# Kernel optimization log

Hardware: AMD Instinct MI355X
Metric: run time of the kernel (lower is better)

The kernel has to match this reference:

```python
import jax, jax.numpy as jnp
import numpy as np

N_NODES = 10000
N_EDGES = 320000
MUL = 32            # multiplicity of each input/output irrep
RADIAL = 8          # edge scalar (radial basis) dim
HID = 64            # fc_neurons widths
NUM_NEIGHBORS = 32.0
MIX = np.pi / 8.0
INV_SQRT2 = 1.0 / np.sqrt(2.0)   # per-path alpha: 2 paths feed each mid irrep
INV_SQRT3 = 1.0 / np.sqrt(3.0)   # w3j(1,1,0) normalization


def setup_inputs() -> dict:
    key = jax.random.key(0)
    ks = jax.random.split(key, 16)
    inp = {
        "node_input": jax.random.normal(ks[0], (N_NODES, 4 * MUL), jnp.float32),  # 32x0e+32x1o flat
        "edge_attr": jax.random.normal(ks[1], (N_EDGES, 4), jnp.float32),          # 1x0e+1x1o (sh l=0,1)
        "edge_scalar_attr": jax.random.uniform(ks[2], (N_EDGES, RADIAL), jnp.float32),
        # first linear: 32x0e+32x1o -> (32x0e+32x1o) + (32x0e+32x1o); columns [:MUL]=conv path, [MUL:]=self path
        "W1_0e": jax.random.normal(ks[3], (MUL, 2 * MUL), jnp.float32),
        "W1_1o": jax.random.normal(ks[4], (MUL, 2 * MUL), jnp.float32),
        # radial MLP
        "W_mlp1": jax.random.normal(ks[5], (RADIAL, HID), jnp.float32),
        "W_mlp2": jax.random.normal(ks[6], (HID, HID), jnp.float32),
        # per-instruction 'uvu' path weights (mul_v = 1 squeezed): shape (HID, MUL)
        "Wp_00": jax.random.normal(ks[7], (HID, MUL), jnp.float32),  # 0e x 0e -> 0e
        "Wp_01": jax.random.normal(ks[8], (HID, MUL), jnp.float32),  # 0e x 1o -> 1o
        "Wp_10": jax.random.normal(ks[9], (HID, MUL), jnp.float32),  # 1o x 0e -> 1o
        "Wp_11": jax.random.normal(ks[10], (HID, MUL), jnp.float32), # 1o x 1o -> 0e
        # final linear: 64x0e+64x1o -> 32x0e+32x1o
        "W2_0e": jax.random.normal(ks[11], (2 * MUL, MUL), jnp.float32),
        "W2_1o": jax.random.normal(ks[12], (2 * MUL, MUL), jnp.float32),
        "edge_src": jax.random.randint(ks[13], (N_EDGES,), 0, N_NODES, jnp.int32),
        "edge_dst": jax.random.randint(ks[14], (N_EDGES,), 0, N_NODES, jnp.int32),
    }
    return inp


def _forward(node_input, edge_attr, edge_scalar_attr,
             W1_0e, W1_1o, W_mlp1, W_mlp2,
             Wp_00, Wp_01, Wp_10, Wp_11, W2_0e, W2_1o,
             edge_src, edge_dst):
    N = node_input.shape[0]
    # split flat node features into irrep blocks: 32x0e (N,32), 32x1o (N,32,3)
    x0 = node_input[:, :MUL]
    x1 = node_input[:, MUL:].reshape(N, MUL, 3)

    # ---- equivariant Linear: input -> input + output (fan-in normalized) ----
    f0 = (x0 @ W1_0e) / np.sqrt(MUL)                           # (N, 2*MUL)
    f1 = jnp.einsum('nui,uw->nwi', x1, W1_1o) / np.sqrt(MUL)   # (N, 2*MUL, 3)
    feat0, self0 = f0[:, :MUL], f0[:, MUL:]
    feat1, self1 = f1[:, :MUL], f1[:, MUL:]

    # ---- gather to edges ----
    e0 = feat0[edge_src]        # (E, MUL)
    e1 = feat1[edge_src]        # (E, MUL, 3)
    ea0 = edge_attr[:, :1]      # (E, 1) 0e
    ea1 = edge_attr[:, 1:4]     # (E, 3) 1o

    # ---- radial MLP -> per-edge per-path weights ----
    h = jax.nn.gelu((edge_scalar_attr @ W_mlp1) / np.sqrt(RADIAL))
    h = jax.nn.gelu((h @ W_mlp2) / np.sqrt(HID))               # (E, HID)
    w00 = h @ Wp_00   # (E, MUL)
    w01 = h @ Wp_01
    w10 = h @ Wp_10
    w11 = h @ Wp_11

    # ---- CG tensor product, 'uvu' mode (mul_v = 1) ----
    out0_a = w00 * e0 * ea0                                   # 0e x 0e -> 0e   (E, MUL)
    out0_b = w11 * jnp.sum(e1 * ea1[:, None, :], -1) * INV_SQRT3  # 1o.1o -> 0e
    out1_a = (w01 * e0)[:, :, None] * ea1[:, None, :]         # 0e x 1o -> 1o   (E, MUL, 3)
    out1_b = (w10[:, :, None] * e1) * ea0[:, :, None]         # 1o x 0e -> 1o
    mid0 = jnp.concatenate([out0_a, out0_b], axis=1) * INV_SQRT2  # (E, 2*MUL)   64x0e
    mid1 = jnp.concatenate([out1_a, out1_b], axis=1) * INV_SQRT2  # (E, 2*MUL, 3) 64x1o

    # ---- scatter-add to destination nodes ----
    n0 = jax.ops.segment_sum(mid0, edge_dst, num_segments=N) / np.sqrt(NUM_NEIGHBORS)
    n1 = jax.ops.segment_sum(mid1, edge_dst, num_segments=N) / np.sqrt(NUM_NEIGHBORS)

    # ---- final equivariant Linear: 64x0e+64x1o -> 32x0e+32x1o ----
    conv0 = (n0 @ W2_0e) / np.sqrt(2 * MUL)                    # (N, MUL)
    conv1 = jnp.einsum('nui,uw->nwi', n1, W2_1o) / np.sqrt(2 * MUL)  # (N, MUL, 3)

    c, s = np.cos(MIX), np.sin(MIX)
    y0 = c * self0 + s * conv0
    y1 = c * self1 + s * conv1
    return jnp.concatenate([y0, y1.reshape(N, MUL * 3)], axis=1)  # (N, 128)


def reference(node_input, edge_attr, edge_scalar_attr,
              W1_0e, W1_1o, W_mlp1, W_mlp2,
              Wp_00, Wp_01, Wp_10, Wp_11, W2_0e, W2_1o,
              edge_src, edge_dst):
    return _forward(node_input, edge_attr, edge_scalar_attr,
                    W1_0e, W1_1o, W_mlp1, W_mlp2,
                    Wp_00, Wp_01, Wp_10, Wp_11, W2_0e, W2_1o,
                    edge_src, edge_dst)
```

## Files before the change

### kernel.cpp

```cpp
#include <hip/hip_runtime.h>

typedef unsigned int uint32;
typedef unsigned short ushrt;
typedef __attribute__((ext_vector_type(4))) float f32x4;
typedef __attribute__((ext_vector_type(16))) float f32x16;
typedef __attribute__((ext_vector_type(2))) float f32x2;
typedef __attribute__((ext_vector_type(8))) _Float16 halfx8;
typedef __attribute__((ext_vector_type(4))) uint32 uint32x4;

#define N_NODES 10000
#define N_EDGES 320000

#define SC_W1      0.17677669529663687f
#define SC_MLP1    0.35355339059327373f
#define SC_MLP2    0.125f
#define INV_SQRT3  0.5773502691896258f
#define COS_MIX    0.9238795325112867f
#define SIN_CONV   0.04783542904563623f

#define WS_FEATP 0
#define I_CNT    1280000
#define I_OFF    1290016
#define U_REC    1300032
#define U_WF     2580032
#define U_WBUF   2587200

__device__ __forceinline__ uint32 f2bf(float x) {
    uint32 u = __float_as_uint(x);
    return (u + 0x7fffu + ((u >> 16) & 1u)) >> 16;
}
__device__ __forceinline__ uint32 pack_bf2(float a, float b) {
    return f2bf(a) | (f2bf(b) << 16);
}
__device__ __forceinline__ uint32 packh2(float a, float b) {
    _Float16 ha = (_Float16)a, hb = (_Float16)b;
    return (uint32)__builtin_bit_cast(unsigned short, ha) |
           ((uint32)__builtin_bit_cast(unsigned short, hb) << 16);
}
__device__ __forceinline__ unsigned short h16(float x) {
    _Float16 h = (_Float16)x;
    return __builtin_bit_cast(unsigned short, h);
}
__device__ __forceinline__ unsigned short pack_fp8_2(float a, float b) {
    return (unsigned short)(__builtin_amdgcn_cvt_pk_fp8_f32(a, b, 0, false) & 0xffff);
}
__device__ __forceinline__ float gelu_fast(float x) {
    float x2 = x * x;
    float z = x * __builtin_fmaf(0.03567740814f, x2, 0.7978845608f);
    float E = __builtin_amdgcn_exp2f(z * -2.885390082f);
    return x * __builtin_amdgcn_rcpf(1.0f + E);
}

#define K1_CNT_BLOCKS  1250
#define K1_PREP_BLOCKS 7
__global__ __launch_bounds__(256) void k1_fused(
        const int* __restrict__ edge_dst, int* __restrict__ cnt,
        const float* __restrict__ Wm1, const float* __restrict__ Wm2,
        const float* __restrict__ Wp00, const float* __restrict__ Wp01,
        const float* __restrict__ Wp10, const float* __restrict__ Wp11,
        uint32* __restrict__ wf) {
    int b = blockIdx.x;
    if (b < K1_CNT_BLOCKS) {
        int e = b * 256 + threadIdx.x;
        atomicAdd(&cnt[edge_dst[e]], 1);
    } else {
        int gid = (b - K1_CNT_BLOCKS) * 256 + threadIdx.x;
        if (gid >= 26 * 64) return;
        int f = gid >> 6, lane = gid & 63;
        int kb = (lane >> 5) * 8;
        int c31 = lane & 31;
        float vals[8];
        if (f < 2) {
            int c = 32 * f + c31;
#pragma unroll
            for (int j = 0; j < 8; ++j) { int k = kb + j; vals[j] = (k < 8) ? Wm1[k * 64 + c] : 0.f; }
        } else if (f < 10) {
            int idx = f - 2, nc = idx >> 2, ks = idx & 3;
            int c = 32 * nc + c31;
#pragma unroll
            for (int j = 0; j < 8; ++j) { int k = 16 * ks + kb + j; vals[j] = Wm2[k * 64 + c]; }
        } else {
            int idx = f - 10, m = idx >> 2, ks = idx & 3;
            const float* W = (m == 0) ? Wp00 : (m == 1) ? Wp01 : (m == 2) ? Wp10 : Wp11;
            float sc = (m == 3) ? 0.125f * INV_SQRT3 : 0.125f;
#pragma unroll
            for (int j = 0; j < 8; ++j) { int k = 16 * ks + kb + j; vals[j] = W[k * 32 + c31] * sc; }
        }
        uint32* o = wf + f * 256 + lane * 4;
#pragma unroll
        for (int w = 0; w < 4; ++w) o[w] = packh2(vals[2 * w], vals[2 * w + 1]);
    }
}

__global__ __launch_bounds__(1024) void csr_scan(const int* __restrict__ cnt,
                                                 int* __restrict__ off) {
    __shared__ int partial[1024];
    int t = threadIdx.x;
    const int CHUNK = 10;
    int base = t * CHUNK;
    int s = 0;
#pragma unroll
    for (int j = 0; j < CHUNK; ++j) {
        int idx = base + j;
        s += (idx < N_NODES) ? cnt[idx] : 0;
    }
    partial[t] = s;
    __syncthreads();
    for (int o = 1; o < 1024; o <<= 1) {
        int v = partial[t];
        int add = (t >= o) ? partial[t - o] : 0;
        __syncthreads();
        partial[t] = v + add;
        __syncthreads();
    }
    int run = (t > 0) ? partial[t - 1] : 0;
    for (int j = 0; j < CHUNK; ++j) {
        int idx = base + j;
        if (idx < N_NODES) {
            off[idx] = run;
            run += cnt[idx];
        }
    }
    if (t == 1023) off[N_NODES] = run;
}

#define MLP_BLOCKS 1250
#define K3_NODE_BLOCKS 2500
__global__ __launch_bounds__(256, 3) void k3_fused(
        const float* __restrict__ edge_scalar, const float* __restrict__ edge_attr,
        const int* __restrict__ src_in, const int* __restrict__ dst_in,
        int* __restrict__ off,
        const uint32* __restrict__ wf,
        uint32* __restrict__ wbuf, uint4* __restrict__ rec,
        const float* __restrict__ x,
        const float* __restrict__ W1_0e, const float* __restrict__ W1_1o,
        float* __restrict__ featp, float* __restrict__ out) {
    __shared__ uint32x4 wfl[26 * 64];
    __shared__ unsigned short sh[4][2048];
    __shared__ float eaxs[4][32];
    __shared__ float xrow[4][128];

    int lane = threadIdx.x & 63;
    int wvq = threadIdx.x >> 6;

    if (blockIdx.x >= MLP_BLOCKS) {
        int node = (blockIdx.x - MLP_BLOCKS) * 4 + wvq;
        float2 v = *(const float2*)(x + (size_t)node * 128 + lane * 2);
        xrow[wvq][lane * 2]     = v.x;
        xrow[wvq][lane * 2 + 1] = v.y;
        __syncthreads();
        const float* sx = xrow[wvq];
        int w = lane;
        float f0 = 0.f, f1x = 0.f, f1y = 0.f, f1z = 0.f;
#pragma unroll
        for (int u = 0; u < 32; ++u) {
            float w0 = W1_0e[u * 64 + w];
            float w1 = W1_1o[u * 64 + w];
            f0  += sx[u] * w0;
            f1x += sx[32 + u * 3 + 0] * w1;
            f1y += sx[32 + u * 3 + 1] * w1;
            f1z += sx[32 + u * 3 + 2] * w1;
        }
        f0 *= SC_W1; f1x *= SC_W1; f1y *= SC_W1; f1z *= SC_W1;
        if (w < 32) {
            featp[node * 128 + w]      = f0;
            featp[node * 128 + 32 + w] = f1x;
            featp[node * 128 + 64 + w] = f1y;
            featp[node * 128 + 96 + w] = f1z;
        } else {
            int ww = w - 32;
            out[node * 128 + ww] = COS_MIX * f0;
            out[node * 128 + 32 + ww * 3 + 0] = COS_MIX * f1x;
            out[node * 128 + 32 + ww * 3 + 1] = COS_MIX * f1y;
            out[node * 128 + 32 + ww * 3 + 2] = COS_MIX * f1z;
        }
        return;
    }

    {
        const uint32x4* s = (const uint32x4*)wf;
        for (int i = threadIdx.x; i < 26 * 64; i += 256) wfl[i] = s[i];
    }
    __syncthreads();

    int wave_id = blockIdx.x * 4 + wvq;
    int l31 = lane & 31;
    int lhi = lane >> 5;

    const f32x16 z16 = {0,0,0,0,0,0,0,0,0,0,0,0,0,0,0,0};
    unsigned short* shw = sh[wvq];
    uint32* obw = (uint32*)shw;
    unsigned short* obw16 = shw;

    for (int g = wave_id; g < N_EDGES / 32; g += MLP_BLOCKS * 4) {
        int e0 = g * 32;

        halfx8 a0 = (halfx8)0;
        if (lane < 32) {
            int e = e0 + lane;
            const float* esp = edge_scalar + (size_t)e * 8;
            float4 p = *(const float4*)esp;
            float4 q = *(const float4*)(esp + 4);
            float4 av = *(const float4*)(edge_attr + (size_t)e * 4);
            int dn = dst_in[e];
            int sn = src_in[e];
            int pos = atomicAdd(&off[dn], 1);
            eaxs[wvq][lane] = av.x;
            uint4 rv;
            rv.x = pack_bf2(av.y, av.z);
            rv.y = __float_as_uint(av.w);
            rv.z = (uint32)e;
            rv.w = (uint32)sn;
            rec[pos] = rv;
            a0[0] = (_Float16)p.x; a0[1] = (_Float16)p.y;
            a0[2] = (_Float16)p.z; a0[3] = (_Float16)p.w;
            a0[4] = (_Float16)q.x; a0[5] = (_Float16)q.y;
            a0[6] = (_Float16)q.z; a0[7] = (_Float16)q.w;
        }

        f32x16 acc1[2];
#pragma unroll
        for (int nc = 0; nc < 2; ++nc) {
            halfx8 bb = __builtin_bit_cast(halfx8, wfl[nc * 64 + lane]);
            acc1[nc] = __builtin_amdgcn_mfma_f32_32x32x16_f16(a0, bb, z16, 0, 0, 0);
        }
#pragma unroll
        for (int nc = 0; nc < 2; ++nc)
#pragma unroll
            for (int reg = 0; reg < 16; ++reg) {
                float gv = gelu_fast(acc1[nc][reg] * SC_MLP1);
                int r = (reg & 3) + 8 * (reg >> 2) + 4 * lhi;
                int ix = r * 64 + 32 * nc + l31;
                shw[ix ^ ((r & 7) << 3)] = h16(gv);
            }
        halfx8 a1[4];
#pragma unroll
        for (int ks = 0; ks < 4; ++ks) {
            int ix = l31 * 64 + 16 * ks + lhi * 8;
            a1[ks] = __builtin_bit_cast(halfx8,
                       *(const uint32x4*)&shw[ix ^ ((lane & 7) << 3)]);
        }

        f32x16 acc2[2];
#pragma unroll
        for (int nc = 0; nc < 2; ++nc) {
            acc2[nc] = z16;
#pragma unroll
            for (int ks = 0; ks < 4; ++ks) {
                halfx8 bb = __builtin_bit_cast(halfx8, wfl[(2 + nc * 4 + ks) * 64 + lane]);
                acc2[nc] = __builtin_amdgcn_mfma_f32_32x32x16_f16(a1[ks], bb, acc2[nc], 0, 0, 0);
            }
        }
#pragma unroll
        for (int nc = 0; nc < 2; ++nc)
#pragma unroll
            for (int reg = 0; reg < 16; ++reg) {
                float gv = gelu_fast(acc2[nc][reg] * SC_MLP2);
                int r = (reg & 3) + 8 * (reg >> 2) + 4 * lhi;
                int ix = r * 64 + 32 * nc + l31;
                shw[ix ^ ((r & 7) << 3)] = h16(gv);
            }
        halfx8 a2[4];
#pragma unroll
        for (int ks = 0; ks < 4; ++ks) {
            int ix = l31 * 64 + 16 * ks + lhi * 8;
            a2[ks] = __builtin_bit_cast(halfx8,
                       *(const uint32x4*)&shw[ix ^ ((lane & 7) << 3)]);
        }

        f32x16 accp[4];
#pragma unroll
        for (int m = 0; m < 4; ++m) {
            accp[m] = z16;
#pragma unroll
            for (int ks = 0; ks < 4; ++ks) {
                halfx8 bb = __builtin_bit_cast(halfx8, wfl[(10 + m * 4 + ks) * 64 + lane]);
                accp[m] = __builtin_amdgcn_mfma_f32_32x32x16_f16(a2[ks], bb, accp[m], 0, 0, 0);
            }
        }

#pragma unroll
        for (int reg = 0; reg < 16; ++reg) {
            int r = (reg & 3) + 8 * (reg >> 2) + 4 * lhi;
            float eax = eaxs[wvq][r];
            obw16[r * 64 + l31]      = pack_fp8_2(accp[0][reg] * eax, accp[1][reg]);
            obw16[r * 64 + 32 + l31] = pack_fp8_2(accp[2][reg] * eax, accp[3][reg]);
        }
#pragma unroll
        for (int pass = 0; pass < 4; ++pass) {
            int r = pass * 8 + (lane >> 3);
            int c4 = (lane & 7) * 4;
            uint32x4 v = *(const uint32x4*)&obw[r * 32 + c4];
            *(uint32x4*)(wbuf + (size_t)(e0 + r) * 32 + c4) = v;
        }
    }
}

__global__ __launch_bounds__(256) void gather(const int* __restrict__ off,
                                              const int* __restrict__ cnt,
                                              const uint4* __restrict__ rec,
                                              const uint32* __restrict__ wbuf,
                                              const float* __restrict__ featp,
                                              const float* __restrict__ W2_0e,
                                              const float* __restrict__ W2_1o,
                                              float* __restrict__ out) {
    int wv = threadIdx.x >> 6;
    int lane = threadIdx.x & 63;
    int node = blockIdx.x * 4 + wv;
    int u = lane & 31;
    int half = lane >> 5;

    int end = __builtin_amdgcn_readfirstlane(off[node]);
    int beg = end - __builtin_amdgcn_readfirstlane(cnt[node]);

    float a0acc = 0.f, a1x = 0.f, a1y = 0.f, a1z = 0.f;
    int offA = u + half * 32, offB = 64 + u, offC = 96 + u;
    const ushrt* wbuf16 = (const ushrt*)wbuf;
    int uslot = (half << 5) + u;

    for (int i0 = beg; i0 < end; i0 += 64) {
        int nn = end - i0;
        if (nn > 64) nn = 64;
        int idx = i0 + ((lane < nn) ? lane : 0);
        uint4 rv = rec[idx];
        int yzv = (int)rv.x, ewv = (int)rv.y, eev = (int)rv.z, svv = (int)rv.w;
        for (int j0 = 0; j0 < nn; j0 += 4) {
            uint32 wl_[4];
            float fa_[4], fb_[4], fc_[4], ey_[4], ez_[4], ew_[4];
#pragma unroll
            for (int t = 0; t < 4; ++t) {
                int j = j0 + t;
                int jc = (j < nn) ? j : nn - 1;
                uint32 yz = (uint32)__builtin_amdgcn_readlane(yzv, jc);
                ey_[t] = __uint_as_float(yz << 16);
                ez_[t] = __uint_as_float(yz & 0xffff0000u);
                ew_[t] = __uint_as_float((uint32)__builtin_amdgcn_readlane(ewv, jc));
                int e  = __builtin_amdgcn_readlane(eev, jc);
                int s  = __builtin_amdgcn_readlane(svv, jc);
                uint32 wl = (uint32)wbuf16[(size_t)e * 64 + uslot];
                wl_[t] = (j < nn) ? wl : 0u;
                const float* fp = featp + (size_t)s * 128;
                fa_[t] = fp[offA];
                fb_[t] = fp[offB];
                fc_[t] = fp[offC];
            }
#pragma unroll
            for (int t = 0; t < 4; ++t) {
                f32x2 wab = __builtin_amdgcn_cvt_pk_f32_fp8((int)wl_[t], false);
                float wa = wab.x;
                float wb = wab.y;
                float va = half ? ey_[t] : 1.0f;
                float vb = half ? ez_[t] : 0.0f;
                float vc = half ? ew_[t] : 0.0f;
                float dot = fa_[t] * va + fb_[t] * vb + fc_[t] * vc;
                float w0s = half ? wb : wa;
                a0acc += w0s * dot;
                float m  = half ? wa : wb * fa_[t];
                float vx = half ? fa_[t] : ey_[t];
                float vy = half ? fb_[t] : ez_[t];
                float vz = half ? fc_[t] : ew_[t];
                a1x += m * vx; a1y += m * vy; a1z += m * vz;
            }
        }
    }

    __shared__ float red[4][256];
    float* r = red[wv];
    int c = (half << 5) + u;
    r[c] = a0acc;
    int b = 64 + c * 3;
    r[b] = a1x; r[b + 1] = a1y; r[b + 2] = a1z;
    __syncthreads();

    if (half == 0) {
        float acc = 0.f;
#pragma unroll 8
        for (int w = 0; w < 64; ++w) acc += r[w] * W2_0e[w * 32 + u];
        int o = node * 128 + u;
        out[o] = out[o] + SIN_CONV * acc;
    } else {
        float c0 = 0.f, c1 = 0.f, c2 = 0.f;
#pragma unroll 8
        for (int w = 0; w < 64; ++w) {
            float bw = W2_1o[w * 32 + u];
            c0 += r[64 + w * 3 + 0] * bw;
            c1 += r[64 + w * 3 + 1] * bw;
            c2 += r[64 + w * 3 + 2] * bw;
        }
        int o = node * 128 + 32 + u * 3;
        out[o + 0] = out[o + 0] + SIN_CONV * c0;
        out[o + 1] = out[o + 1] + SIN_CONV * c1;
        out[o + 2] = out[o + 2] + SIN_CONV * c2;
    }
}

extern "C" void kernel_launch(void* const* d_in, const int* in_sizes, int n_in,
                              void* d_out, int out_size, void* d_ws, size_t ws_size,
                              hipStream_t stream) {
    const float* node_input  = (const float*)d_in[0];
    const float* edge_attr   = (const float*)d_in[1];
    const float* edge_scalar = (const float*)d_in[2];
    const float* W1_0e       = (const float*)d_in[3];
    const float* W1_1o       = (const float*)d_in[4];
    const float* W_mlp1      = (const float*)d_in[5];
    const float* W_mlp2      = (const float*)d_in[6];
    const float* Wp00        = (const float*)d_in[7];
    const float* Wp01        = (const float*)d_in[8];
    const float* Wp10        = (const float*)d_in[9];
    const float* Wp11        = (const float*)d_in[10];
    const float* W2_0e       = (const float*)d_in[11];
    const float* W2_1o       = (const float*)d_in[12];
    const int*   edge_src    = (const int*)d_in[13];
    const int*   edge_dst    = (const int*)d_in[14];
    float* ws   = (float*)d_ws;
    int*   wsI  = (int*)d_ws;
    uint32* wsU = (uint32*)d_ws;
    uint4* recp = (uint4*)(wsU + U_REC);
    float* outp = (float*)d_out;

    hipMemsetAsync(wsI + I_CNT, 0, (N_NODES + 1) * sizeof(int), stream);

    k1_fused<<<K1_CNT_BLOCKS + K1_PREP_BLOCKS, 256, 0, stream>>>(
        edge_dst, wsI + I_CNT,
        W_mlp1, W_mlp2, Wp00, Wp01, Wp10, Wp11, wsU + U_WF);
    csr_scan<<<1, 1024, 0, stream>>>(wsI + I_CNT, wsI + I_OFF);
    k3_fused<<<MLP_BLOCKS + K3_NODE_BLOCKS, 256, 0, stream>>>(
        edge_scalar, edge_attr, edge_src, edge_dst, wsI + I_OFF,
        wsU + U_WF, wsU + U_WBUF, recp,
        node_input, W1_0e, W1_1o, ws + WS_FEATP, outp);
    gather<<<N_NODES / 4, 256, 0, stream>>>(wsI + I_OFF, wsI + I_CNT, recp,
                                            wsU + U_WBUF, ws + WS_FEATP,
                                            W2_0e, W2_1o, outp);
}
```

Measured before the change: 114.0 us.

## Fold CSR scan into fused edge kernel and split record scatter into own kernel

The separate single-block CSR scan launch is removed; block 0 of the fused edge/node kernel now runs the prefix scan with 256 threads while the other blocks do the node linear and the edge MLP. Because the offsets are not ready during that kernel, the atomic slot claim and record write move into a new rec_scatter kernel launched afterwards. This overlaps the serial scan with useful work and removes one launch. In exchange it adds a kernel launch and re-reads edge_attr, and the scan block with 40-element chunks per thread may become a long tail.

```diff
diff --git a/kernel.cpp b/kernel.cpp
--- a/kernel.cpp
+++ b/kernel.cpp
@@ -92,46 +92,13 @@
     }
 }
 
-__global__ __launch_bounds__(1024) void csr_scan(const int* __restrict__ cnt,
-                                                 int* __restrict__ off) {
-    __shared__ int partial[1024];
-    int t = threadIdx.x;
-    const int CHUNK = 10;
-    int base = t * CHUNK;
-    int s = 0;
-#pragma unroll
-    for (int j = 0; j < CHUNK; ++j) {
-        int idx = base + j;
-        s += (idx < N_NODES) ? cnt[idx] : 0;
-    }
-    partial[t] = s;
-    __syncthreads();
-    for (int o = 1; o < 1024; o <<= 1) {
-        int v = partial[t];
-        int add = (t >= o) ? partial[t - o] : 0;
-        __syncthreads();
-        partial[t] = v + add;
-        __syncthreads();
-    }
-    int run = (t > 0) ? partial[t - 1] : 0;
-    for (int j = 0; j < CHUNK; ++j) {
-        int idx = base + j;
-        if (idx < N_NODES) {
-            off[idx] = run;
-            run += cnt[idx];
-        }
-    }
-    if (t == 1023) off[N_NODES] = run;
-}
-
+#define K3_NODE_BLOCKS 2500
 #define MLP_BLOCKS 1250
-#define K3_NODE_BLOCKS 2500
 __global__ __launch_bounds__(256, 3) void k3_fused(
         const float* __restrict__ edge_scalar, const float* __restrict__ edge_attr,
-        const int* __restrict__ src_in, const int* __restrict__ dst_in,
-        int* __restrict__ off,
+        const int* __restrict__ cnt, int* __restrict__ off,
         const uint32* __restrict__ wf,
-        uint32* __restrict__ wbuf, uint4* __restrict__ rec,
+        uint32* __restrict__ wbuf,
         const float* __restrict__ x,
         const float* __restrict__ W1_0e, const float* __restrict__ W1_1o,
         float* __restrict__ featp, float* __restrict__ out) {
@@ -139,12 +106,44 @@
     __shared__ unsigned short sh[4][2048];
     __shared__ float eaxs[4][32];
     __shared__ float xrow[4][128];
+    __shared__ int   partial[256];
 
     int lane = threadIdx.x & 63;
     int wvq = threadIdx.x >> 6;
 
-    if (blockIdx.x >= MLP_BLOCKS) {
-        int node = (blockIdx.x - MLP_BLOCKS) * 4 + wvq;
+    if (blockIdx.x == 0) {
+        int t = threadIdx.x;
+        const int CHUNK = 40;
+        int base = t * CHUNK;
+        int s = 0;
+#pragma unroll
+        for (int j = 0; j < CHUNK; ++j) {
+            int idx = base + j;
+            s += (idx < N_NODES) ? cnt[idx] : 0;
+        }
+        partial[t] = s;
+        __syncthreads();
+        for (int o = 1; o < 256; o <<= 1) {
+            int v = partial[t];
+            int add = (t >= o) ? partial[t - o] : 0;
+            __syncthreads();
+            partial[t] = v + add;
+            __syncthreads();
+        }
+        int run = (t > 0) ? partial[t - 1] : 0;
+        for (int j = 0; j < CHUNK; ++j) {
+            int idx = base + j;
+            if (idx < N_NODES) {
+                off[idx] = run;
+                run += cnt[idx];
+            }
+        }
+        if (t == 255) off[N_NODES] = run;
+        return;
+    }
+
+    if (blockIdx.x <= K3_NODE_BLOCKS) {
+        int node = (blockIdx.x - 1) * 4 + wvq;
         float2 v = *(const float2*)(x + (size_t)node * 128 + lane * 2);
         xrow[wvq][lane * 2]     = v.x;
         xrow[wvq][lane * 2 + 1] = v.y;
@@ -183,7 +182,7 @@
     }
     __syncthreads();
 
-    int wave_id = blockIdx.x * 4 + wvq;
+    int wave_id = (blockIdx.x - 1 - K3_NODE_BLOCKS) * 4 + wvq;
     int l31 = lane & 31;
     int lhi = lane >> 5;
 
@@ -201,17 +200,7 @@
             const float* esp = edge_scalar + (size_t)e * 8;
             float4 p = *(const float4*)esp;
             float4 q = *(const float4*)(esp + 4);
-            float4 av = *(const float4*)(edge_attr + (size_t)e * 4);
-            int dn = dst_in[e];
-            int sn = src_in[e];
-            int pos = atomicAdd(&off[dn], 1);
-            eaxs[wvq][lane] = av.x;
-            uint4 rv;
-            rv.x = pack_bf2(av.y, av.z);
-            rv.y = __float_as_uint(av.w);
-            rv.z = (uint32)e;
-            rv.w = (uint32)sn;
-            rec[pos] = rv;
+            eaxs[wvq][lane] = edge_attr[(size_t)e * 4];
             a0[0] = (_Float16)p.x; a0[1] = (_Float16)p.y;
             a0[2] = (_Float16)p.z; a0[3] = (_Float16)p.w;
             a0[4] = (_Float16)q.x; a0[5] = (_Float16)q.y;
@@ -294,6 +283,23 @@
             *(uint32x4*)(wbuf + (size_t)(e0 + r) * 32 + c4) = v;
         }
     }
+}
+
+__global__ __launch_bounds__(256) void rec_scatter(
+        const int* __restrict__ src_in, const int* __restrict__ dst_in,
+        const float* __restrict__ edge_attr,
+        int* __restrict__ off, uint4* __restrict__ rec) {
+    int e = blockIdx.x * 256 + threadIdx.x;
+    float4 av = *(const float4*)(edge_attr + (size_t)e * 4);
+    int sn = src_in[e];
+    int dn = dst_in[e];
+    int pos = atomicAdd(&off[dn], 1);
+    uint4 rv;
+    rv.x = pack_bf2(av.y, av.z);
+    rv.y = __float_as_uint(av.w);
+    rv.z = (uint32)e;
+    rv.w = (uint32)sn;
+    rec[pos] = rv;
 }
 
 __global__ __launch_bounds__(256) void gather(const int* __restrict__ off,
@@ -423,11 +429,12 @@
     k1_fused<<<K1_CNT_BLOCKS + K1_PREP_BLOCKS, 256, 0, stream>>>(
         edge_dst, wsI + I_CNT,
         W_mlp1, W_mlp2, Wp00, Wp01, Wp10, Wp11, wsU + U_WF);
-    csr_scan<<<1, 1024, 0, stream>>>(wsI + I_CNT, wsI + I_OFF);
-    k3_fused<<<MLP_BLOCKS + K3_NODE_BLOCKS, 256, 0, stream>>>(
-        edge_scalar, edge_attr, edge_src, edge_dst, wsI + I_OFF,
-        wsU + U_WF, wsU + U_WBUF, recp,
+    k3_fused<<<1 + K3_NODE_BLOCKS + MLP_BLOCKS, 256, 0, stream>>>(
+        edge_scalar, edge_attr, wsI + I_CNT, wsI + I_OFF,
+        wsU + U_WF, wsU + U_WBUF,
         node_input, W1_0e, W1_1o, ws + WS_FEATP, outp);
+    rec_scatter<<<1250, 256, 0, stream>>>(edge_src, edge_dst, edge_attr,
+                                          wsI + I_OFF, recp);
     gather<<<N_NODES / 4, 256, 0, stream>>>(wsI + I_OFF, wsI + I_CNT, recp,
                                             wsU + U_WBUF, ws + WS_FEATP,
                                             W2_0e, W2_1o, outp);
```

New measurement: 124.8 us. +9.5%, slower.
